# Optimization experiments

Measured on AMD Instinct MI355X. Metric: run time of the kernel, lower is better.

The kernel has to match this reference:

```python
import jax, jax.numpy as jnp
import numpy as np

B, S, HID, H = 4, 2048, 1024, 16
D = HID // H  # dim per head


def setup_inputs() -> dict:
    key = jax.random.key(0)
    ks = jax.random.split(key, 7)
    inp = {
        "q": jax.random.normal(ks[0], (B, S, HID), dtype=jnp.float32),
        "k": jax.random.normal(ks[1], (B, S, HID), dtype=jnp.float32),
        "v": jax.random.normal(ks[2], (B, S, HID), dtype=jnp.float32),
        # Linear weights stored as (in, out); applied as x @ W. use_bias=False.
        "Wq": jax.random.normal(ks[3], (HID, HID), dtype=jnp.float32) * (1.0 / np.sqrt(HID)),
        "Wk": jax.random.normal(ks[4], (HID, HID), dtype=jnp.float32) * (1.0 / np.sqrt(HID)),
        "Wv": jax.random.normal(ks[5], (HID, HID), dtype=jnp.float32) * (1.0 / np.sqrt(HID)),
        "Wo": jax.random.normal(ks[6], (HID, HID), dtype=jnp.float32) * (1.0 / np.sqrt(HID)),
    }
    return inp


def reference(q, k, v, Wq, Wk, Wv, Wo):
    scale = 1.0 / jnp.sqrt(jnp.float32(D))
    # QKV projections, then split hidden into (H, D) heads (same layout as transpose_qkv)
    Q = (q @ Wq).reshape(B, S, H, D)
    K = (k @ Wk).reshape(B, S, H, D)
    V = (v @ Wv).reshape(B, S, H, D)
    # scaled dot-product attention: full [B,H,S,S] score matrix, softmax over keys
    attn_w = jnp.einsum("bqhd,bkhd->bhqk", Q, K) * scale
    attn_w = jax.nn.softmax(attn_w, axis=-1)
    # dropout rate is 0 (eval-mode / deterministic)
    O = jnp.einsum("bhqk,bkhd->bqhd", attn_w, V).reshape(B, S, HID)
    return O @ Wo
```

## Files before the change

kernel.cpp:

```cpp
#include <hip/hip_runtime.h>


typedef __attribute__((ext_vector_type(8))) short short8;
typedef __attribute__((ext_vector_type(4))) float float4v;

#if __has_builtin(__builtin_amdgcn_exp2f)
#define EXP2F(x) __builtin_amdgcn_exp2f(x)
#else
#define EXP2F(x) exp2f(x)
#endif

__device__ __forceinline__ unsigned short f2b(float x) {
  return (unsigned short)((__float_as_uint(x) + 0x8000u) >> 16);
}
__device__ __forceinline__ unsigned pk2f(float a, float b) {
  unsigned ua = __float_as_uint(a) + 0x8000u;
  unsigned ub = __float_as_uint(b) + 0x8000u;
  return __builtin_amdgcn_perm(ub, ua, 0x07060302);
}

typedef __attribute__((address_space(3))) unsigned int lds_uint;
typedef const __attribute__((address_space(1))) unsigned int gbl_uint;
__device__ __forceinline__ void stage16(const unsigned short* g, unsigned short* l) {
#if __has_builtin(__builtin_amdgcn_global_load_lds)
  __builtin_amdgcn_global_load_lds((gbl_uint*)g, (lds_uint*)l, 16, 0, 0);
#else
  *(uint4*)l = *(const uint4*)g;
#endif
}

__global__ __launch_bounds__(256) void conv_qkv(const float* __restrict__ q,
                                                const float* __restrict__ k,
                                                const float* __restrict__ v,
                                                unsigned short* __restrict__ ws,
                                                float qscale) {
  const int z = blockIdx.y;
  const float* src = z == 0 ? q : (z == 1 ? k : v);
  unsigned short* dst = ws + (size_t)z * 8388608;
  const float s = z == 0 ? qscale : 1.0f;
  size_t i = ((size_t)blockIdx.x * 256 + threadIdx.x) * 8;
  float4v a = *(const float4v*)(src + i);
  float4v b = *(const float4v*)(src + i + 4);
  uint4 o;
  o.x = pk2f(a.x * s, a.y * s);
  o.y = pk2f(a.z * s, a.w * s);
  o.z = pk2f(b.x * s, b.y * s);
  o.w = pk2f(b.z * s, b.w * s);
  *(uint4*)(dst + i) = o;
}

__global__ __launch_bounds__(256) void wtrans(const float* __restrict__ Wq,
                                              const float* __restrict__ Wk,
                                              const float* __restrict__ Wv,
                                              const float* __restrict__ Wo,
                                              unsigned short* __restrict__ Wt) {
  __shared__ float tile[32][33];
  const float* W = blockIdx.z == 0 ? Wq : blockIdx.z == 1 ? Wk
                   : blockIdx.z == 2 ? Wv : Wo;
  unsigned short* T = Wt + (size_t)blockIdx.z * 1048576;
  const int tx = threadIdx.x & 31, ty = threadIdx.x >> 5;
  const int k0 = blockIdx.y * 32, n0 = blockIdx.x * 32;
#pragma unroll
  for (int i = 0; i < 4; i++)
    tile[ty + 8 * i][tx] = W[(size_t)(k0 + ty + 8 * i) * 1024 + n0 + tx];
  __syncthreads();
#pragma unroll
  for (int i = 0; i < 4; i++)
    T[(size_t)(n0 + ty + 8 * i) * 1024 + k0 + tx] = f2b(tile[tx][ty + 8 * i]);
}

template <int MODE, bool SWAP>
__global__ __launch_bounds__(256, 2) void gemm_bt(const unsigned short* __restrict__ A,
                                                  const unsigned short* __restrict__ Bt,
                                                  void* __restrict__ Cg) {
  __shared__ __align__(16) unsigned short As[128 * 64];
  __shared__ __align__(16) unsigned short Bs[128 * 64];
  const int tid = threadIdx.x;
  const int lane = tid & 63;
  const int w = tid >> 6;
  const int quad = lane >> 4, col = lane & 15;
  const int wm = w >> 1, wn = w & 1;
  const int lin = blockIdx.x;
  const int xcd = lin & 7, grp = lin >> 3;
  const int m0 = ((grp & 7) * 8 + xcd) * 128;
  const int n0 = (grp >> 3) * 128;
  const int rA = lane >> 3, cA = lane & 7;

  float4v acc[4][4] = {};

  for (int k0 = 0; k0 < 1024; k0 += 64) {
    __syncthreads();
#pragma unroll
    for (int j = 0; j < 4; j++) {
      const int row = w * 32 + j * 8 + rA;
      stage16(A + (unsigned)(m0 + row) * 1024 + k0 + ((cA ^ rA) * 8),
              &As[row * 64 + cA * 8]);
      stage16(Bt + (unsigned)(n0 + row) * 1024 + k0 + ((cA ^ rA) * 8),
              &Bs[row * 64 + cA * 8]);
    }
    __syncthreads();

#pragma unroll
    for (int ks = 0; ks < 2; ks++) {
      short8 af[4], bf[4];
#pragma unroll
      for (int mi = 0; mi < 4; mi++) {
        int row = wm * 64 + mi * 16 + col;
        af[mi] = *(const short8*)&As[row * 64 + (((ks * 4 + quad) ^ (col & 7)) * 8)];
      }
#pragma unroll
      for (int ni = 0; ni < 4; ni++) {
        int row = wn * 64 + ni * 16 + col;
        bf[ni] = *(const short8*)&Bs[row * 64 + (((ks * 4 + quad) ^ (col & 7)) * 8)];
      }
#pragma unroll
      for (int mi = 0; mi < 4; mi++)
#pragma unroll
        for (int ni = 0; ni < 4; ni++) {
          if (SWAP)
            acc[ni][mi] = __builtin_amdgcn_mfma_f32_16x16x32_bf16(
                bf[ni], af[mi], acc[ni][mi], 0, 0, 0);
          else
            acc[mi][ni] = __builtin_amdgcn_mfma_f32_16x16x32_bf16(
                af[mi], bf[ni], acc[mi][ni], 0, 0, 0);
        }
    }
  }

  if (MODE == 0) {
#pragma unroll
    for (int ni = 0; ni < 4; ni++) {
      const int cg = n0 + wn * 64 + ni * 16 + quad * 4;
      const int h = cg >> 6, dlo = cg & 63;
#pragma unroll
      for (int mi = 0; mi < 4; mi++) {
        const int tok = m0 + wm * 64 + mi * 16 + col;
        const int b = tok >> 11, s = tok & 2047;
        uint2 pk;
        pk.x = pk2f(acc[ni][mi][0], acc[ni][mi][1]);
        pk.y = pk2f(acc[ni][mi][2], acc[ni][mi][3]);
        *(uint2*)((unsigned short*)Cg +
                  ((unsigned)((b * 16 + h) * 2048 + s) * 64 + dlo)) = pk;
      }
    }
  } else if (MODE == 1) {
#pragma unroll
    for (int mi = 0; mi < 4; mi++) {
      const int tok = m0 + wm * 64 + mi * 16 + quad * 4;
      const int b = tok >> 11, s = tok & 2047;
#pragma unroll
      for (int ni = 0; ni < 4; ni++) {
        const int cg = n0 + wn * 64 + ni * 16 + col;
        const int h = cg >> 6, d = cg & 63;
        uint2 pk;
        pk.x = pk2f(acc[mi][ni][0], acc[mi][ni][1]);
        pk.y = pk2f(acc[mi][ni][2], acc[mi][ni][3]);
        *(uint2*)((unsigned short*)Cg +
                  ((unsigned)((b * 16 + h) * 64 + d) * 2048 + s)) = pk;
      }
    }
  } else {
#pragma unroll
    for (int mi = 0; mi < 4; mi++) {
      const int row = m0 + wm * 64 + mi * 16 + quad * 4;
#pragma unroll
      for (int ni = 0; ni < 4; ni++) {
        const int cg = n0 + wn * 64 + ni * 16 + col;
#pragma unroll
        for (int r = 0; r < 4; r++)
          ((float*)Cg)[(unsigned)(row + r) * 1024 + cg] = acc[mi][ni][r];
      }
    }
  }
}

#define PSTR 160
__global__ __launch_bounds__(256, 2) void attn_kernel(
    const unsigned short* __restrict__ Qb, const unsigned short* __restrict__ Kb,
    const unsigned short* __restrict__ Vt, unsigned short* __restrict__ Ob) {
  __shared__ __align__(16) unsigned short K_lds[128 * 64];
  __shared__ __align__(16) unsigned short V_lds[64 * 128];
  __shared__ __align__(16) unsigned short P_lds[128 * PSTR];
  __shared__ float den_lds[128];

  const int tid = threadIdx.x;
  const int lane = tid & 63;
  const int w = tid >> 6;
  const int quad = lane >> 4, col = lane & 15;
  const int wq = w >> 1, wk = w & 1;
  const int lin = blockIdx.x;
  const int bh = ((lin >> 3) & 7) * 8 + (lin & 7);
  const int qt = lin >> 6;

  const unsigned short* Kbase = Kb + (size_t)bh * (2048 * 64);
  const unsigned short* Vbase = Vt + (size_t)bh * (64 * 2048);

  short8 qf[4][2];
#pragma unroll
  for (int qi = 0; qi < 4; qi++)
#pragma unroll
    for (int ks = 0; ks < 2; ks++) {
      int s = qt * 128 + wq * 64 + qi * 16 + col;
      qf[qi][ks] = *(const short8*)(Qb + ((size_t)bh * 2048 + s) * 64 + ks * 32 + quad * 8);
    }

  float4v oacc[2][4] = {};
  float dens[4] = {};

  if (tid < 128) den_lds[tid] = 0.f;

  const int rK = lane >> 3, cK = lane & 7;
  const int rV = lane >> 4, cV = lane & 15;

  for (int kt = 0; kt < 16; kt++) {
    const int s0 = kt * 128;
    __syncthreads();
#pragma unroll
    for (int j = 0; j < 4; j++) {
      const int rowK = w * 32 + j * 8 + rK;
      stage16(Kbase + (unsigned)(s0 + rowK) * 64 + ((cK ^ rK) * 8),
              &K_lds[rowK * 64 + cK * 8]);
      const int rowV = w * 16 + j * 4 + rV;
      stage16(Vbase + (unsigned)rowV * 2048 + s0 + (((cV ^ (rowV & 15)) & 15) * 8),
              &V_lds[rowV * 128 + cV * 8]);
    }
    __syncthreads();

    float4v sacc[4][4] = {};
    short8 kf[4][2];
#pragma unroll
    for (int ki = 0; ki < 4; ki++)
#pragma unroll
      for (int ks = 0; ks < 2; ks++) {
        int row = wk * 64 + ki * 16 + col;
        kf[ki][ks] = *(const short8*)&K_lds[row * 64 +
                                            (((ks * 4 + quad) ^ (col & 7)) * 8)];
      }
#pragma unroll
    for (int ki = 0; ki < 4; ki++)
#pragma unroll
      for (int qi = 0; qi < 4; qi++)
#pragma unroll
        for (int ks = 0; ks < 2; ks++)
          sacc[ki][qi] = __builtin_amdgcn_mfma_f32_16x16x32_bf16(
              kf[ki][ks], qf[qi][ks], sacc[ki][qi], 0, 0, 0);

#pragma unroll
    for (int ki = 0; ki < 4; ki++) {
      const int c = wk * 8 + ki * 2 + (quad >> 1);
      const int hh = quad & 1;
#pragma unroll
      for (int qi = 0; qi < 4; qi++) {
        const int q = wq * 64 + qi * 16 + col;
        float p0 = EXP2F(sacc[ki][qi][0]);
        float p1 = EXP2F(sacc[ki][qi][1]);
        float p2 = EXP2F(sacc[ki][qi][2]);
        float p3 = EXP2F(sacc[ki][qi][3]);
        dens[qi] += (p0 + p1) + (p2 + p3);
        uint2 pk;
        pk.x = pk2f(p0, p1);
        pk.y = pk2f(p2, p3);
        *(uint2*)&P_lds[q * PSTR + ((c ^ col) & 15) * 8 + hh * 4] = pk;
      }
    }
    __syncthreads();

#pragma unroll
    for (int ks = 0; ks < 4; ks++) {
      short8 pf[4], vf[2];
#pragma unroll
      for (int mi = 0; mi < 4; mi++) {
        int row = wq * 64 + mi * 16 + col;
        pf[mi] = *(const short8*)&P_lds[row * PSTR + ((((ks * 4 + quad) ^ col) & 15) * 8)];
      }
#pragma unroll
      for (int nv = 0; nv < 2; nv++) {
        int row = wk * 32 + nv * 16 + col;
        vf[nv] = *(const short8*)&V_lds[row * 128 + ((((ks * 4 + quad) ^ col) & 15) * 8)];
      }
#pragma unroll
      for (int nv = 0; nv < 2; nv++)
#pragma unroll
        for (int mi = 0; mi < 4; mi++)
          oacc[nv][mi] = __builtin_amdgcn_mfma_f32_16x16x32_bf16(
              vf[nv], pf[mi], oacc[nv][mi], 0, 0, 0);
    }
  }

#pragma unroll
  for (int qi = 0; qi < 4; qi++) {
    float v = dens[qi];
    v += __shfl_xor(v, 16);
    v += __shfl_xor(v, 32);
    if (lane < 16) atomicAdd(&den_lds[wq * 64 + qi * 16 + col], v);
  }
  __syncthreads();

  const int b = bh >> 4, h = bh & 15;
#pragma unroll
  for (int mi = 0; mi < 4; mi++) {
    const int srow = qt * 128 + wq * 64 + mi * 16 + col;
    const float rd = 1.f / den_lds[wq * 64 + mi * 16 + col];
    unsigned base = (unsigned)(b * 2048 + srow) * 1024 + h * 64;
#pragma unroll
    for (int nv = 0; nv < 2; nv++) {
      const int d0 = wk * 32 + nv * 16 + quad * 4;
      uint2 pk;
      pk.x = pk2f(oacc[nv][mi][0] * rd, oacc[nv][mi][1] * rd);
      pk.y = pk2f(oacc[nv][mi][2] * rd, oacc[nv][mi][3] * rd);
      *(uint2*)(Ob + base + d0) = pk;
    }
  }
}

extern "C" void kernel_launch(void* const* d_in, const int* in_sizes, int n_in,
                              void* d_out, int out_size, void* d_ws, size_t ws_size,
                              hipStream_t stream) {
  const float* q = (const float*)d_in[0];
  const float* k = (const float*)d_in[1];
  const float* v = (const float*)d_in[2];
  const float* Wq = (const float*)d_in[3];
  const float* Wk = (const float*)d_in[4];
  const float* Wv = (const float*)d_in[5];
  const float* Wo = (const float*)d_in[6];

  unsigned short* ws = (unsigned short*)d_ws;
  unsigned short* qb = ws;
  unsigned short* kb = ws + 8388608;
  unsigned short* vb = ws + 16777216;
  unsigned short* Qb = ws + 25165824;
  unsigned short* Kb = ws + 33554432;
  unsigned short* Vt = ws + 41943040;
  unsigned short* Wt = ws + 50331648;

  dim3 blk(256);
  const float qscale = 0.18033688011112042f;

  conv_qkv<<<dim3(4096, 3), blk, 0, stream>>>(q, k, v, ws, qscale);
  wtrans<<<dim3(32, 32, 4), blk, 0, stream>>>(Wq, Wk, Wv, Wo, Wt);

  gemm_bt<0, true><<<dim3(512), blk, 0, stream>>>(qb, Wt + 0 * 1048576, Qb);
  gemm_bt<0, true><<<dim3(512), blk, 0, stream>>>(kb, Wt + 1 * 1048576, Kb);
  gemm_bt<1, false><<<dim3(512), blk, 0, stream>>>(vb, Wt + 2 * 1048576, Vt);

  attn_kernel<<<dim3(1024), blk, 0, stream>>>(Qb, Kb, Vt, qb );

  gemm_bt<2, false><<<dim3(512), blk, 0, stream>>>(qb , Wt + 3 * 1048576,
                                                   (float*)d_out);
}
```

Measured before the change: 346.9 us.

## Rewrite attention kernel with 32x32 MFMA, register-resident P, and double-buffered K/V

The attention kernel moves from 16x16x32 to 32x32x16 bf16 MFMA, with each wave owning 32 full query rows. The probability tile stays in registers, rearranged by a cross-half lane swap (permlane32_swap where available), instead of a round trip through LDS. K/V tiles shrink to 64 keys and are double-buffered so the next tile's global-to-LDS load overlaps compute, with one barrier per iteration instead of three. The row denominator is now reduced within a wave, removing the LDS atomics, at the cost of higher register pressure and a layout shuffle per tile.

```diff
diff --git a/kernel.cpp b/kernel.cpp
--- a/kernel.cpp
+++ b/kernel.cpp
@@ -3,6 +3,8 @@
 
 typedef __attribute__((ext_vector_type(8))) short short8;
 typedef __attribute__((ext_vector_type(4))) float float4v;
+typedef __attribute__((ext_vector_type(16))) float float16v;
+typedef __attribute__((ext_vector_type(2))) unsigned int uint2v;
 
 #if __has_builtin(__builtin_amdgcn_exp2f)
 #define EXP2F(x) __builtin_amdgcn_exp2f(x)
@@ -174,143 +176,133 @@
   }
 }
 
-#define PSTR 160
 __global__ __launch_bounds__(256, 2) void attn_kernel(
     const unsigned short* __restrict__ Qb, const unsigned short* __restrict__ Kb,
     const unsigned short* __restrict__ Vt, unsigned short* __restrict__ Ob) {
-  __shared__ __align__(16) unsigned short K_lds[128 * 64];
-  __shared__ __align__(16) unsigned short V_lds[64 * 128];
-  __shared__ __align__(16) unsigned short P_lds[128 * PSTR];
-  __shared__ float den_lds[128];
+  __shared__ __align__(16) unsigned short K_lds[2][64 * 64];
+  __shared__ __align__(16) unsigned short V_lds[2][64 * 64];
 
   const int tid = threadIdx.x;
   const int lane = tid & 63;
   const int w = tid >> 6;
-  const int quad = lane >> 4, col = lane & 15;
-  const int wq = w >> 1, wk = w & 1;
+  const int l5 = lane & 31, hi = lane >> 5;
+
   const int lin = blockIdx.x;
   const int bh = ((lin >> 3) & 7) * 8 + (lin & 7);
   const int qt = lin >> 6;
 
   const unsigned short* Kbase = Kb + (size_t)bh * (2048 * 64);
   const unsigned short* Vbase = Vt + (size_t)bh * (64 * 2048);
-
-  short8 qf[4][2];
-#pragma unroll
-  for (int qi = 0; qi < 4; qi++)
-#pragma unroll
-    for (int ks = 0; ks < 2; ks++) {
-      int s = qt * 128 + wq * 64 + qi * 16 + col;
-      qf[qi][ks] = *(const short8*)(Qb + ((size_t)bh * 2048 + s) * 64 + ks * 32 + quad * 8);
-    }
-
-  float4v oacc[2][4] = {};
-  float dens[4] = {};
-
-  if (tid < 128) den_lds[tid] = 0.f;
-
-  const int rK = lane >> 3, cK = lane & 7;
-  const int rV = lane >> 4, cV = lane & 15;
-
-  for (int kt = 0; kt < 16; kt++) {
-    const int s0 = kt * 128;
+  const int q0 = qt * 128 + w * 32;
+
+  short8 qf[4];
+#pragma unroll
+  for (int c = 0; c < 4; c++)
+    qf[c] = *(const short8*)(Qb + ((size_t)bh * 2048 + q0 + l5) * 64 + c * 16 + hi * 8);
+
+  float16v oacc[2] = {};
+  float denp[4] = {};
+
+  const int sr = lane >> 3, sc = lane & 7;
+
+  auto STAGE = [&](int b, int kt) {
+    const int s0 = kt * 64;
+#pragma unroll
+    for (int j = 0; j < 2; j++) {
+      const int row = w * 16 + j * 8 + sr;
+      stage16(Kbase + (unsigned)(s0 + row) * 64 + ((sc ^ sr) * 8),
+              &K_lds[b][row * 64 + sc * 8]);
+      stage16(Vbase + (unsigned)row * 2048 + s0 + ((sc ^ sr) * 8),
+              &V_lds[b][row * 64 + sc * 8]);
+    }
+  };
+
+  STAGE(0, 0);
+  __syncthreads();
+
+  int cur = 0;
+  for (int kt = 0; kt < 32; kt++) {
+    if (kt < 31) STAGE(cur ^ 1, kt + 1);
+
+    const unsigned short* Kl = &K_lds[cur][0];
+    const unsigned short* Vl = &V_lds[cur][0];
+
+    float16v sacc[2] = {};
+    __builtin_amdgcn_s_setprio(1);
+#pragma unroll
+    for (int t = 0; t < 2; t++)
+#pragma unroll
+      for (int c = 0; c < 4; c++) {
+        short8 kf = *(const short8*)&Kl[(t * 32 + l5) * 64 +
+                                        (((c * 2 + hi) ^ (l5 & 7)) * 8)];
+        sacc[t] = __builtin_amdgcn_mfma_f32_32x32x16_bf16(kf, qf[c], sacc[t], 0, 0, 0);
+      }
+    __builtin_amdgcn_s_setprio(0);
+
+    short8 pf[4];
+#pragma unroll
+    for (int t = 0; t < 2; t++) {
+#pragma unroll
+      for (int r = 0; r < 16; r++) {
+        float p = EXP2F(sacc[t][r]);
+        sacc[t][r] = p;
+        denp[r & 3] += p;
+      }
+#pragma unroll
+      for (int half = 0; half < 2; half++) {
+        const int k0 = half * 8;
+        unsigned P0 = pk2f(sacc[t][k0 + 0], sacc[t][k0 + 1]);
+        unsigned P1 = pk2f(sacc[t][k0 + 2], sacc[t][k0 + 3]);
+        unsigned P2 = pk2f(sacc[t][k0 + 4], sacc[t][k0 + 5]);
+        unsigned P3 = pk2f(sacc[t][k0 + 6], sacc[t][k0 + 7]);
+        unsigned u0, u1, u2, u3;
+#if __has_builtin(__builtin_amdgcn_permlane32_swap)
+        uint2v a02 = __builtin_amdgcn_permlane32_swap(P0, P2, false, false);
+        uint2v a13 = __builtin_amdgcn_permlane32_swap(P1, P3, false, false);
+        u0 = a02[0]; u2 = a02[1];
+        u1 = a13[0]; u3 = a13[1];
+#else
+        unsigned p0s = __shfl_xor((int)P0, 32), p2s = __shfl_xor((int)P2, 32);
+        unsigned p1s = __shfl_xor((int)P1, 32), p3s = __shfl_xor((int)P3, 32);
+        u0 = hi ? p2s : P0; u2 = hi ? P2 : p0s;
+        u1 = hi ? p3s : P1; u3 = hi ? P3 : p1s;
+#endif
+        union { unsigned u[4]; short8 s; } cv;
+        cv.u[0] = u0; cv.u[1] = u1; cv.u[2] = u2; cv.u[3] = u3;
+        pf[t * 2 + half] = cv.s;
+      }
+    }
+
+    __builtin_amdgcn_s_setprio(1);
+#pragma unroll
+    for (int dt = 0; dt < 2; dt++)
+#pragma unroll
+      for (int kc = 0; kc < 4; kc++) {
+        short8 vf = *(const short8*)&Vl[(dt * 32 + l5) * 64 +
+                                        (((kc * 2 + hi) ^ (l5 & 7)) * 8)];
+        oacc[dt] = __builtin_amdgcn_mfma_f32_32x32x16_bf16(vf, pf[kc], oacc[dt], 0, 0, 0);
+      }
+    __builtin_amdgcn_s_setprio(0);
+
     __syncthreads();
-#pragma unroll
-    for (int j = 0; j < 4; j++) {
-      const int rowK = w * 32 + j * 8 + rK;
-      stage16(Kbase + (unsigned)(s0 + rowK) * 64 + ((cK ^ rK) * 8),
-              &K_lds[rowK * 64 + cK * 8]);
-      const int rowV = w * 16 + j * 4 + rV;
-      stage16(Vbase + (unsigned)rowV * 2048 + s0 + (((cV ^ (rowV & 15)) & 15) * 8),
-              &V_lds[rowV * 128 + cV * 8]);
-    }
-    __syncthreads();
-
-    float4v sacc[4][4] = {};
-    short8 kf[4][2];
-#pragma unroll
-    for (int ki = 0; ki < 4; ki++)
-#pragma unroll
-      for (int ks = 0; ks < 2; ks++) {
-        int row = wk * 64 + ki * 16 + col;
-        kf[ki][ks] = *(const short8*)&K_lds[row * 64 +
-                                            (((ks * 4 + quad) ^ (col & 7)) * 8)];
-      }
-#pragma unroll
-    for (int ki = 0; ki < 4; ki++)
-#pragma unroll
-      for (int qi = 0; qi < 4; qi++)
-#pragma unroll
-        for (int ks = 0; ks < 2; ks++)
-          sacc[ki][qi] = __builtin_amdgcn_mfma_f32_16x16x32_bf16(
-              kf[ki][ks], qf[qi][ks], sacc[ki][qi], 0, 0, 0);
-
-#pragma unroll
-    for (int ki = 0; ki < 4; ki++) {
-      const int c = wk * 8 + ki * 2 + (quad >> 1);
-      const int hh = quad & 1;
-#pragma unroll
-      for (int qi = 0; qi < 4; qi++) {
-        const int q = wq * 64 + qi * 16 + col;
-        float p0 = EXP2F(sacc[ki][qi][0]);
-        float p1 = EXP2F(sacc[ki][qi][1]);
-        float p2 = EXP2F(sacc[ki][qi][2]);
-        float p3 = EXP2F(sacc[ki][qi][3]);
-        dens[qi] += (p0 + p1) + (p2 + p3);
-        uint2 pk;
-        pk.x = pk2f(p0, p1);
-        pk.y = pk2f(p2, p3);
-        *(uint2*)&P_lds[q * PSTR + ((c ^ col) & 15) * 8 + hh * 4] = pk;
-      }
-    }
-    __syncthreads();
-
-#pragma unroll
-    for (int ks = 0; ks < 4; ks++) {
-      short8 pf[4], vf[2];
-#pragma unroll
-      for (int mi = 0; mi < 4; mi++) {
-        int row = wq * 64 + mi * 16 + col;
-        pf[mi] = *(const short8*)&P_lds[row * PSTR + ((((ks * 4 + quad) ^ col) & 15) * 8)];
-      }
-#pragma unroll
-      for (int nv = 0; nv < 2; nv++) {
-        int row = wk * 32 + nv * 16 + col;
-        vf[nv] = *(const short8*)&V_lds[row * 128 + ((((ks * 4 + quad) ^ col) & 15) * 8)];
-      }
-#pragma unroll
-      for (int nv = 0; nv < 2; nv++)
-#pragma unroll
-        for (int mi = 0; mi < 4; mi++)
-          oacc[nv][mi] = __builtin_amdgcn_mfma_f32_16x16x32_bf16(
-              vf[nv], pf[mi], oacc[nv][mi], 0, 0, 0);
-    }
+    cur ^= 1;
   }
 
-#pragma unroll
-  for (int qi = 0; qi < 4; qi++) {
-    float v = dens[qi];
-    v += __shfl_xor(v, 16);
-    v += __shfl_xor(v, 32);
-    if (lane < 16) atomicAdd(&den_lds[wq * 64 + qi * 16 + col], v);
-  }
-  __syncthreads();
+  float den = (denp[0] + denp[1]) + (denp[2] + denp[3]);
+  den += __shfl_xor(den, 32);
+  const float rd = 1.f / den;
 
   const int b = bh >> 4, h = bh & 15;
-#pragma unroll
-  for (int mi = 0; mi < 4; mi++) {
-    const int srow = qt * 128 + wq * 64 + mi * 16 + col;
-    const float rd = 1.f / den_lds[wq * 64 + mi * 16 + col];
-    unsigned base = (unsigned)(b * 2048 + srow) * 1024 + h * 64;
-#pragma unroll
-    for (int nv = 0; nv < 2; nv++) {
-      const int d0 = wk * 32 + nv * 16 + quad * 4;
+  const unsigned obase = (unsigned)(b * 2048 + q0 + l5) * 1024 + h * 64;
+#pragma unroll
+  for (int dt = 0; dt < 2; dt++)
+#pragma unroll
+    for (int g = 0; g < 4; g++) {
       uint2 pk;
-      pk.x = pk2f(oacc[nv][mi][0] * rd, oacc[nv][mi][1] * rd);
-      pk.y = pk2f(oacc[nv][mi][2] * rd, oacc[nv][mi][3] * rd);
-      *(uint2*)(Ob + base + d0) = pk;
-    }
-  }
+      pk.x = pk2f(oacc[dt][4 * g + 0] * rd, oacc[dt][4 * g + 1] * rd);
+      pk.y = pk2f(oacc[dt][4 * g + 2] * rd, oacc[dt][4 * g + 3] * rd);
+      *(uint2*)(Ob + obase + dt * 32 + 8 * g + 4 * hi) = pk;
+    }
 }
 
 extern "C" void kernel_launch(void* const* d_in, const int* in_sizes, int n_in,
```

Result: no change. 341.3 us (-1.6%).
